# Kernel tuning notes

Hardware: AMD Instinct MI355X
Metric: run time of the kernel (lower is better)

Reference implementation:

```python
import jax, jax.numpy as jnp
import numpy as np

N_NODES = 50000
DIM = 128
N_EDGES = 800000
N_UID = 4096
ORDER = 3
LN_EPS = 1e-5


def setup_inputs() -> dict:
    key = jax.random.key(0)
    ks = jax.random.split(key, 6)
    scale = 1.0 / np.sqrt(DIM)
    embedding = jax.random.normal(ks[0], (N_NODES, DIM), jnp.float32) * np.sqrt(2.0 / DIM)  # kaiming-ish
    W = jax.random.normal(ks[1], (ORDER, DIM, DIM), jnp.float32) * scale
    b = jnp.zeros((ORDER, DIM), jnp.float32)
    gamma = jnp.ones((ORDER, DIM), jnp.float32)
    beta = jnp.zeros((ORDER, DIM), jnp.float32)
    src = jax.random.randint(ks[2], (N_EDGES,), 0, N_NODES, jnp.int32)
    dst = jax.random.randint(ks[3], (N_EDGES,), 0, N_NODES, jnp.int32)
    uid = jax.random.randint(ks[4], (N_UID,), 0, N_NODES, jnp.int32)
    return {"embedding": embedding, "W": W, "b": b, "gamma": gamma,
            "beta": beta, "src": src, "dst": dst, "uid": uid}


def _layer_norm(x, g, bta):
    mu = jnp.mean(x, axis=-1, keepdims=True)
    var = jnp.var(x, axis=-1, keepdims=True)
    return (x - mu) * jax.lax.rsqrt(var + LN_EPS) * g + bta


def reference(embedding, W, b, gamma, beta, src, dst, uid):
    # in-degree per destination node (DGL 'gcn' aggregator uses in_degrees)
    deg = jax.ops.segment_sum(jnp.ones((src.shape[0],), embedding.dtype), dst,
                              num_segments=N_NODES)  # [N]
    inv = (1.0 / (deg + 1.0))[:, None]  # [N,1]
    feats = embedding
    for i in range(ORDER):
        # gather source features, scatter-sum into destinations
        neigh = jax.ops.segment_sum(feats[src], dst, num_segments=N_NODES)  # [N,D]
        h = (neigh + feats) * inv                    # gcn-style mean incl. self
        h = jnp.einsum('nd,ed->ne', h, W[i]) + b[i]  # fc_neigh
        feats = jax.nn.elu(_layer_norm(h, gamma[i], beta[i]))
    return feats[uid]  # [N_UID, D]
```

## Files before the change

kernel.cpp:

```cpp
#include <hip/hip_runtime.h>
#include <math.h>

typedef unsigned int   uint;
typedef unsigned short ushort;

#define N_NODES 50000
#define DIM     128
#define N_EDGES 800000
#define N_UID   4096
#define LN_EPS  1e-5f
#define RST     132
#define XST     136
#define NBUCK   196
#define PCHUNK  4096
#define DBINS   128

typedef __attribute__((ext_vector_type(8))) short bf16x8;
typedef __attribute__((ext_vector_type(4))) float f32x4;
typedef __attribute__((ext_vector_type(4))) uint  u32x4;

__device__ __forceinline__ float bf_lo(uint u) { return __builtin_bit_cast(float, u << 16); }
__device__ __forceinline__ float bf_hi(uint u) { return __builtin_bit_cast(float, u & 0xffff0000u); }
__device__ __forceinline__ uint pack_bf16(float a, float b) {
    uint ua = __builtin_bit_cast(uint, a);
    uint ub = __builtin_bit_cast(uint, b);
    uint ra = (ua + 0x7fffu + ((ua >> 16) & 1u)) >> 16;
    uint rb = (ub + 0x7fffu + ((ub >> 16) & 1u)) >> 16;
    return ra | (rb << 16);
}

__global__ __launch_bounds__(256) void cvthist_kernel(const float* __restrict__ emb, ushort* __restrict__ E,
                                                      const float* __restrict__ W, ushort* __restrict__ WB,
                                                      const int* __restrict__ dst, int* __restrict__ bhist) {
    __shared__ int h[256];
    const int t = threadIdx.x;
    h[t] = 0;
    __syncthreads();
    const int gsz = gridDim.x * 256;
    for (int i = blockIdx.x * 256 + t; i < N_NODES * DIM / 4; i += gsz) {
        const float4 v = ((const float4*)emb)[i];
        uint2 p;
        p.x = pack_bf16(v.x, v.y);
        p.y = pack_bf16(v.z, v.w);
        ((uint2*)E)[i] = p;
    }
    {
        const int i = blockIdx.x * 256 + t;
        if (i < 3 * DIM * DIM / 4) {
            const float4 v = ((const float4*)W)[i];
            uint2 p;
            p.x = pack_bf16(v.x, v.y);
            p.y = pack_bf16(v.z, v.w);
            ((uint2*)WB)[i] = p;
        }
    }
    for (int e = blockIdx.x * 256 + t; e < N_EDGES; e += gsz)
        atomicAdd(&h[dst[e] >> 8], 1);
    __syncthreads();
    if (t < NBUCK && h[t]) atomicAdd(&bhist[t], h[t]);
}

__global__ __launch_bounds__(256) void part_kernel(const int* __restrict__ src, const int* __restrict__ dst,
                                                   const int* __restrict__ bhist, int* __restrict__ bcur,
                                                   int2* __restrict__ pak) {
    __shared__ int sc[256];
    __shared__ int h[256];
    __shared__ int base[256];
    __shared__ int cur[256];
    const int t = threadIdx.x;
    const int v = (t < NBUCK) ? bhist[t] : 0;
    sc[t] = v;
    h[t] = 0; cur[t] = 0;
    __syncthreads();
    for (int o = 1; o < 256; o <<= 1) {
        int x = (t >= o) ? sc[t - o] : 0;
        __syncthreads();
        sc[t] += x;
        __syncthreads();
    }
    const int excl = sc[t] - v;
    const int e0 = blockIdx.x * PCHUNK;
    const int e1 = min(e0 + PCHUNK, N_EDGES);
    for (int i = e0 + t; i < e1; i += 256)
        atomicAdd(&h[dst[i] >> 8], 1);
    __syncthreads();
    if (t < NBUCK && h[t]) base[t] = excl + atomicAdd(&bcur[t], h[t]);
    __syncthreads();
    for (int i = e0 + t; i < e1; i += 256) {
        const int s = src[i], d = dst[i];
        const int b = d >> 8;
        const int q = atomicAdd(&cur[b], 1);
        pak[base[b] + q] = make_int2(s, d);
    }
}

__global__ __launch_bounds__(256) void bucket_kernel(const int2* __restrict__ pak, const int* __restrict__ bhist,
                                                     int* __restrict__ off, int* __restrict__ csr,
                                                     int* __restrict__ dhist) {
    __shared__ int sc[256];
    __shared__ int cnt[256];
    __shared__ int pos[256];
    __shared__ int dh[DBINS];
    const int b = blockIdx.x, t = threadIdx.x;
    const int bv = (t < NBUCK) ? bhist[t] : 0;
    sc[t] = bv;
    cnt[t] = 0;
    if (t < DBINS) dh[t] = 0;
    __syncthreads();
    for (int o = 1; o < 256; o <<= 1) {
        int x = (t >= o) ? sc[t - o] : 0;
        __syncthreads();
        sc[t] += x;
        __syncthreads();
    }
    const int e0 = (b == 0) ? 0 : sc[b - 1];
    const int e1 = sc[b];
    const int m = e1 - e0;
    for (int i = t; i < m; i += 256) atomicAdd(&cnt[pak[e0 + i].y & 255], 1);
    __syncthreads();
    const int c = cnt[t];
    pos[t] = c;
    __syncthreads();
    for (int o = 1; o < 256; o <<= 1) {
        int x = (t >= o) ? pos[t - o] : 0;
        __syncthreads();
        pos[t] += x;
        __syncthreads();
    }
    const int excl = pos[t] - c;
    const int node = b * 256 + t;
    if (node < N_NODES) {
        off[node] = e0 + excl;
        atomicAdd(&dh[min(c, DBINS - 1)], 1);
    }
    if (b == 0 && t == 0) off[N_NODES] = N_EDGES;
    __syncthreads();
    if (t < DBINS && dh[t]) atomicAdd(&dhist[t], dh[t]);
    pos[t] = excl;
    __syncthreads();
    for (int i = t; i < m; i += 256) {
        const int2 p = pak[e0 + i];
        const int q = atomicAdd(&pos[p.y & 255], 1);
        csr[e0 + q] = p.x;
    }
}

__global__ __launch_bounds__(256) void dscat_kernel(const int* __restrict__ off, const int* __restrict__ dhist,
                                                    int* __restrict__ dcur, int* __restrict__ perm) {
    __shared__ int sc[DBINS];
    __shared__ int dv[DBINS];
    __shared__ int lh[DBINS];
    __shared__ int lbase[DBINS];
    __shared__ int lcur[DBINS];
    const int b = blockIdx.x, t = threadIdx.x;
    if (t < DBINS) { lh[t] = 0; lcur[t] = 0; }
    __syncthreads();
    const int node = b * 256 + t;
    int bin = -1;
    if (node < N_NODES) {
        const int deg = off[node + 1] - off[node];
        bin = min(deg, DBINS - 1);
        atomicAdd(&lh[bin], 1);
    }
    __syncthreads();
    if (t < DBINS) { dv[t] = dhist[t]; sc[t] = dv[t]; }
    __syncthreads();
    for (int o = 1; o < DBINS; o <<= 1) {
        int x = (t >= o && t < DBINS) ? sc[t - o] : 0;
        __syncthreads();
        if (t < DBINS) sc[t] += x;
        __syncthreads();
    }
    if (t < DBINS) {
        const int excl = sc[t] - dv[t];
        if (lh[t]) lbase[t] = excl + atomicAdd(&dcur[t], lh[t]);
    }
    __syncthreads();
    if (node < N_NODES) {
        const int q = atomicAdd(&lcur[bin], 1);
        perm[lbase[bin] + q] = node;
    }
}

template <bool OUT_BF16, bool PERMOUT>
__global__ __launch_bounds__(512) void layer_kernel(
    const ushort* __restrict__ fin, void* __restrict__ fout,
    const int* __restrict__ off, const int* __restrict__ csr,
    const int* __restrict__ nodemap, const ushort* __restrict__ wb,
    const float* __restrict__ bias, const float* __restrict__ gamma,
    const float* __restrict__ beta, int nrows)
{
    __shared__ ushort xs[32 * XST];
    __shared__ float  ys[32 * RST];
    __shared__ int    nid[32];
    const int t = threadIdx.x;
    const int rows = blockIdx.x * 32;

    {
        const int lx   = t & 15;
        const int st   = t >> 4;
        const int slot = rows + st;
        const bool valid = slot < nrows;
        const int n  = valid ? (nodemap ? nodemap[slot] : slot) : 0;
        if (lx == 0) nid[st] = n;
        const int d0 = off[n];
        int d1 = off[n + 1];
        if (!valid) d1 = d0;
        const int deg = d1 - d0;

        float a[8];
        {
            const uint4 q = ((const uint4*)(fin + (size_t)n * DIM))[lx];
            a[0]=bf_lo(q.x); a[1]=bf_hi(q.x); a[2]=bf_lo(q.y); a[3]=bf_hi(q.y);
            a[4]=bf_lo(q.z); a[5]=bf_hi(q.z); a[6]=bf_lo(q.w); a[7]=bf_hi(q.w);
        }

        const int nfull = deg >> 3;
        int e = d0;
        int id[8];
        if (nfull > 0) {
            #pragma unroll
            for (int k = 0; k < 8; ++k) id[k] = csr[e + k];
        }
        for (int r = 0; r < nfull; ++r) {
            uint4 v[8];
            #pragma unroll
            for (int k = 0; k < 8; ++k)
                v[k] = ((const uint4*)(fin + (size_t)id[k] * DIM))[lx];
            int idn[8];
            if (r + 1 < nfull) {
                #pragma unroll
                for (int k = 0; k < 8; ++k) idn[k] = csr[e + 8 + k];
            }
            #pragma unroll
            for (int k = 0; k < 8; ++k) {
                a[0] += bf_lo(v[k].x); a[1] += bf_hi(v[k].x);
                a[2] += bf_lo(v[k].y); a[3] += bf_hi(v[k].y);
                a[4] += bf_lo(v[k].z); a[5] += bf_hi(v[k].z);
                a[6] += bf_lo(v[k].w); a[7] += bf_hi(v[k].w);
            }
            if (r + 1 < nfull) {
                #pragma unroll
                for (int k = 0; k < 8; ++k) id[k] = idn[k];
            }
            e += 8;
        }
        if (e < d1) {
            const int last = d1 - 1;
            int   idt[8];
            float m[8];
            #pragma unroll
            for (int k = 0; k < 8; ++k) {
                const int ee = e + k;
                idt[k] = csr[(ee <= last) ? ee : last];
                m[k]   = (ee <= last) ? 1.0f : 0.0f;
            }
            uint4 v[8];
            #pragma unroll
            for (int k = 0; k < 8; ++k)
                v[k] = ((const uint4*)(fin + (size_t)idt[k] * DIM))[lx];
            #pragma unroll
            for (int k = 0; k < 8; ++k) {
                a[0] = fmaf(m[k], bf_lo(v[k].x), a[0]); a[1] = fmaf(m[k], bf_hi(v[k].x), a[1]);
                a[2] = fmaf(m[k], bf_lo(v[k].y), a[2]); a[3] = fmaf(m[k], bf_hi(v[k].y), a[3]);
                a[4] = fmaf(m[k], bf_lo(v[k].z), a[4]); a[5] = fmaf(m[k], bf_hi(v[k].z), a[5]);
                a[6] = fmaf(m[k], bf_lo(v[k].w), a[6]); a[7] = fmaf(m[k], bf_hi(v[k].w), a[7]);
            }
        }

        const float iv = 1.0f / (float)(deg + 1);
        uint4 p;
        p.x = pack_bf16(a[0] * iv, a[1] * iv);
        p.y = pack_bf16(a[2] * iv, a[3] * iv);
        p.z = pack_bf16(a[4] * iv, a[5] * iv);
        p.w = pack_bf16(a[6] * iv, a[7] * iv);
        *((uint4*)(xs + st * XST + lx * 8)) = p;
    }
    __syncthreads();

    {
        const int wave = t >> 6, lane = t & 63;
        const int row_off = (wave >> 2) * 16;
        const int col_off = (wave & 3) * 32;
        const int lm   = lane & 15;
        const int quad = lane >> 4;
        f32x4 acc[2] = {f32x4{0,0,0,0}, f32x4{0,0,0,0}};
        const ushort* xrow = xs + (row_off + lm) * XST + quad * 8;
        const ushort* __restrict__ wrow = wb + (size_t)(col_off + lm) * DIM + quad * 8;
        #pragma unroll
        for (int kk = 0; kk < 4; ++kk) {
            const bf16x8 af = __builtin_bit_cast(bf16x8, *(const u32x4*)(xrow + kk * 32));
            #pragma unroll
            for (int c = 0; c < 2; ++c) {
                const bf16x8 bf = __builtin_bit_cast(bf16x8,
                    *(const u32x4*)(wrow + (size_t)c * 16 * DIM + kk * 32));
                acc[c] = __builtin_amdgcn_mfma_f32_16x16x32_bf16(af, bf, acc[c], 0, 0, 0);
            }
        }
        #pragma unroll
        for (int c = 0; c < 2; ++c) {
            #pragma unroll
            for (int r = 0; r < 4; ++r)
                ys[(row_off + quad * 4 + r) * RST + col_off + c * 16 + lm] = acc[c][r];
        }
    }
    __syncthreads();

    {
        const int r   = t >> 4;
        const int seg = t & 15;
        const int db  = seg * 8;
        const float* yr = ys + r * RST + db;
        float vs[8];
        {
            const float4 y0 = ((const float4*)yr)[0];
            const float4 y1 = ((const float4*)yr)[1];
            const float4 b0 = ((const float4*)(bias + db))[0];
            const float4 b1 = ((const float4*)(bias + db))[1];
            vs[0] = y0.x + b0.x; vs[1] = y0.y + b0.y; vs[2] = y0.z + b0.z; vs[3] = y0.w + b0.w;
            vs[4] = y1.x + b1.x; vs[5] = y1.y + b1.y; vs[6] = y1.z + b1.z; vs[7] = y1.w + b1.w;
        }
        float s1 = 0.0f, s2 = 0.0f;
        #pragma unroll
        for (int i = 0; i < 8; ++i) { s1 += vs[i]; s2 += vs[i] * vs[i]; }
        #pragma unroll
        for (int m = 1; m < 16; m <<= 1) {
            s1 += __shfl_xor(s1, m);
            s2 += __shfl_xor(s2, m);
        }
        const float mu  = s1 * (1.0f / 128.0f);
        const float var = s2 * (1.0f / 128.0f) - mu * mu;
        const float rs  = rsqrtf(var + LN_EPS);
        float ov[8];
        {
            const float4 g0 = ((const float4*)(gamma + db))[0];
            const float4 g1 = ((const float4*)(gamma + db))[1];
            const float4 t0 = ((const float4*)(beta + db))[0];
            const float4 t1 = ((const float4*)(beta + db))[1];
            float z;
            z = (vs[0] - mu) * rs * g0.x + t0.x; ov[0] = (z > 0.0f) ? z : expm1f(z);
            z = (vs[1] - mu) * rs * g0.y + t0.y; ov[1] = (z > 0.0f) ? z : expm1f(z);
            z = (vs[2] - mu) * rs * g0.z + t0.z; ov[2] = (z > 0.0f) ? z : expm1f(z);
            z = (vs[3] - mu) * rs * g0.w + t0.w; ov[3] = (z > 0.0f) ? z : expm1f(z);
            z = (vs[4] - mu) * rs * g1.x + t1.x; ov[4] = (z > 0.0f) ? z : expm1f(z);
            z = (vs[5] - mu) * rs * g1.y + t1.y; ov[5] = (z > 0.0f) ? z : expm1f(z);
            z = (vs[6] - mu) * rs * g1.z + t1.z; ov[6] = (z > 0.0f) ? z : expm1f(z);
            z = (vs[7] - mu) * rs * g1.w + t1.w; ov[7] = (z > 0.0f) ? z : expm1f(z);
        }
        const int slot3 = rows + r;
        if (slot3 < nrows) {
            const int nout = PERMOUT ? nid[r] : slot3;
            if (OUT_BF16) {
                uint4 p;
                p.x = pack_bf16(ov[0], ov[1]);
                p.y = pack_bf16(ov[2], ov[3]);
                p.z = pack_bf16(ov[4], ov[5]);
                p.w = pack_bf16(ov[6], ov[7]);
                *((uint4*)((ushort*)fout + (size_t)nout * DIM + db)) = p;
            } else {
                float* op = (float*)fout + (size_t)nout * DIM + db;
                ((float4*)op)[0] = make_float4(ov[0], ov[1], ov[2], ov[3]);
                ((float4*)op)[1] = make_float4(ov[4], ov[5], ov[6], ov[7]);
            }
        }
    }
}

extern "C" void kernel_launch(void* const* d_in, const int* in_sizes, int n_in,
                              void* d_out, int out_size, void* d_ws, size_t ws_size,
                              hipStream_t stream) {
    const float* emb   = (const float*)d_in[0];
    const float* W     = (const float*)d_in[1];
    const float* bias  = (const float*)d_in[2];
    const float* gamma = (const float*)d_in[3];
    const float* beta  = (const float*)d_in[4];
    const int*   src   = (const int*)d_in[5];
    const int*   dst   = (const int*)d_in[6];
    const int*   uid   = (const int*)d_in[7];

    ushort* E     = (ushort*)d_ws;
    ushort* A     = E + (size_t)N_NODES * DIM;
    ushort* B     = A + (size_t)N_NODES * DIM;
    ushort* WB    = B + (size_t)N_NODES * DIM;
    int*    off   = (int*)(WB + 3 * DIM * DIM);
    int*    aux   = off + (N_NODES + 4);
    int*    bhist = aux;
    int*    bcur  = aux + 256;
    int*    dhist = aux + 512;
    int*    dcur  = aux + 640;
    int*    perm  = aux + 768;
    int2*   pak   = (int2*)(perm + N_NODES);
    int*    csr   = (int*)(pak + N_EDGES);

    hipMemsetAsync(aux, 0, 768 * sizeof(int), stream);
    cvthist_kernel<<<512, 256, 0, stream>>>(emb, E, W, WB, dst, bhist);
    part_kernel<<<(N_EDGES + PCHUNK - 1) / PCHUNK, 256, 0, stream>>>(src, dst, bhist, bcur, pak);
    bucket_kernel<<<NBUCK, 256, 0, stream>>>(pak, bhist, off, csr, dhist);
    dscat_kernel<<<NBUCK, 256, 0, stream>>>(off, dhist, dcur, perm);

    const int lblk = (N_NODES + 31) / 32;
    layer_kernel<true, true><<<lblk, 512, 0, stream>>>(E, A, off, csr, perm, WB,
                                                       bias, gamma, beta, N_NODES);
    layer_kernel<true, true><<<lblk, 512, 0, stream>>>(A, B, off, csr, perm, WB + DIM * DIM,
                                                       bias + DIM, gamma + DIM, beta + DIM, N_NODES);
    layer_kernel<false, false><<<N_UID / 32, 512, 0, stream>>>(B, (float*)d_out, off, csr, uid,
                                                               WB + 2 * DIM * DIM, bias + 2 * DIM,
                                                               gamma + 2 * DIM, beta + 2 * DIM, N_UID);
}
```

Measured before the change: 233.7 us.

## Replace degree-sorted node permutation with edge-balanced per-block aggregation

Drops the degree histogram and permutation kernel and processes nodes in natural order. Within each 32-node block, edges are split evenly across 32 sub-groups, each binary-searches its starting node and flushes partial sums into shared memory with atomics. This aims to remove the extra dscat launch and the scattered permuted reads and writes while still balancing per-row gather work. In exchange it adds LDS atomics, a zeroing pass and a binary search, and blocks whose nodes have very different degrees stay unbalanced against each other.

```diff
diff --git a/kernel.cpp b/kernel.cpp
--- a/kernel.cpp
+++ b/kernel.cpp
@@ -13,7 +13,6 @@
 #define XST     136
 #define NBUCK   196
 #define PCHUNK  4096
-#define DBINS   128
 
 typedef __attribute__((ext_vector_type(8))) short bf16x8;
 typedef __attribute__((ext_vector_type(4))) float f32x4;
@@ -95,17 +94,14 @@
 }
 
 __global__ __launch_bounds__(256) void bucket_kernel(const int2* __restrict__ pak, const int* __restrict__ bhist,
-                                                     int* __restrict__ off, int* __restrict__ csr,
-                                                     int* __restrict__ dhist) {
+                                                     int* __restrict__ off, int* __restrict__ csr) {
     __shared__ int sc[256];
     __shared__ int cnt[256];
     __shared__ int pos[256];
-    __shared__ int dh[DBINS];
     const int b = blockIdx.x, t = threadIdx.x;
     const int bv = (t < NBUCK) ? bhist[t] : 0;
     sc[t] = bv;
     cnt[t] = 0;
-    if (t < DBINS) dh[t] = 0;
     __syncthreads();
     for (int o = 1; o < 256; o <<= 1) {
         int x = (t >= o) ? sc[t - o] : 0;
@@ -129,13 +125,9 @@
     }
     const int excl = pos[t] - c;
     const int node = b * 256 + t;
-    if (node < N_NODES) {
-        off[node] = e0 + excl;
-        atomicAdd(&dh[min(c, DBINS - 1)], 1);
-    }
+    if (node < N_NODES) off[node] = e0 + excl;
     if (b == 0 && t == 0) off[N_NODES] = N_EDGES;
     __syncthreads();
-    if (t < DBINS && dh[t]) atomicAdd(&dhist[t], dh[t]);
     pos[t] = excl;
     __syncthreads();
     for (int i = t; i < m; i += 256) {
@@ -145,136 +137,94 @@
     }
 }
 
-__global__ __launch_bounds__(256) void dscat_kernel(const int* __restrict__ off, const int* __restrict__ dhist,
-                                                    int* __restrict__ dcur, int* __restrict__ perm) {
-    __shared__ int sc[DBINS];
-    __shared__ int dv[DBINS];
-    __shared__ int lh[DBINS];
-    __shared__ int lbase[DBINS];
-    __shared__ int lcur[DBINS];
-    const int b = blockIdx.x, t = threadIdx.x;
-    if (t < DBINS) { lh[t] = 0; lcur[t] = 0; }
-    __syncthreads();
-    const int node = b * 256 + t;
-    int bin = -1;
-    if (node < N_NODES) {
-        const int deg = off[node + 1] - off[node];
-        bin = min(deg, DBINS - 1);
-        atomicAdd(&lh[bin], 1);
-    }
-    __syncthreads();
-    if (t < DBINS) { dv[t] = dhist[t]; sc[t] = dv[t]; }
-    __syncthreads();
-    for (int o = 1; o < DBINS; o <<= 1) {
-        int x = (t >= o && t < DBINS) ? sc[t - o] : 0;
-        __syncthreads();
-        if (t < DBINS) sc[t] += x;
-        __syncthreads();
-    }
-    if (t < DBINS) {
-        const int excl = sc[t] - dv[t];
-        if (lh[t]) lbase[t] = excl + atomicAdd(&dcur[t], lh[t]);
-    }
-    __syncthreads();
-    if (node < N_NODES) {
-        const int q = atomicAdd(&lcur[bin], 1);
-        perm[lbase[bin] + q] = node;
-    }
-}
-
-template <bool OUT_BF16, bool PERMOUT>
-__global__ __launch_bounds__(512) void layer_kernel(
-    const ushort* __restrict__ fin, void* __restrict__ fout,
+__global__ __launch_bounds__(512) void layerbal_kernel(
+    const ushort* __restrict__ fin, ushort* __restrict__ fout,
     const int* __restrict__ off, const int* __restrict__ csr,
-    const int* __restrict__ nodemap, const ushort* __restrict__ wb,
-    const float* __restrict__ bias, const float* __restrict__ gamma,
-    const float* __restrict__ beta, int nrows)
+    const ushort* __restrict__ wb, const float* __restrict__ bias,
+    const float* __restrict__ gamma, const float* __restrict__ beta, int nrows)
 {
     __shared__ ushort xs[32 * XST];
     __shared__ float  ys[32 * RST];
-    __shared__ int    nid[32];
+    __shared__ int    noff[33];
     const int t = threadIdx.x;
     const int rows = blockIdx.x * 32;
-
-    {
-        const int lx   = t & 15;
-        const int st   = t >> 4;
-        const int slot = rows + st;
-        const bool valid = slot < nrows;
-        const int n  = valid ? (nodemap ? nodemap[slot] : slot) : 0;
-        if (lx == 0) nid[st] = n;
-        const int d0 = off[n];
-        int d1 = off[n + 1];
-        if (!valid) d1 = d0;
-        const int deg = d1 - d0;
-
-        float a[8];
-        {
-            const uint4 q = ((const uint4*)(fin + (size_t)n * DIM))[lx];
-            a[0]=bf_lo(q.x); a[1]=bf_hi(q.x); a[2]=bf_lo(q.y); a[3]=bf_hi(q.y);
-            a[4]=bf_lo(q.z); a[5]=bf_hi(q.z); a[6]=bf_lo(q.w); a[7]=bf_hi(q.w);
-        }
-
-        const int nfull = deg >> 3;
-        int e = d0;
-        int id[8];
-        if (nfull > 0) {
-            #pragma unroll
-            for (int k = 0; k < 8; ++k) id[k] = csr[e + k];
-        }
-        for (int r = 0; r < nfull; ++r) {
-            uint4 v[8];
-            #pragma unroll
-            for (int k = 0; k < 8; ++k)
-                v[k] = ((const uint4*)(fin + (size_t)id[k] * DIM))[lx];
-            int idn[8];
-            if (r + 1 < nfull) {
+    const int nvalid = min(32, nrows - rows);
+
+    for (int i = t; i < 32 * RST; i += 512) ys[i] = 0.0f;
+    if (t <= nvalid) noff[t] = off[rows + t];
+    __syncthreads();
+
+    {
+        const int lx = t & 15;
+        const int st = t >> 4;
+        const int e0 = noff[0], e1 = noff[nvalid];
+        const int per = ((e1 - e0) + 31) >> 5;
+        const int s0 = e0 + st * per;
+        const int s1 = min(s0 + per, e1);
+        if (s0 < s1) {
+            int lo = 0, hi = nvalid - 1;
+            while (lo < hi) {
+                const int mid = (lo + hi + 1) >> 1;
+                if (noff[mid] <= s0) lo = mid; else hi = mid - 1;
+            }
+            int p  = lo;
+            int nb = noff[p + 1];
+            float acc[8] = {0, 0, 0, 0, 0, 0, 0, 0};
+            for (int e = s0; e < s1; e += 8) {
+                const int cnt = min(8, s1 - e);
+                int id[8];
                 #pragma unroll
-                for (int k = 0; k < 8; ++k) idn[k] = csr[e + 8 + k];
-            }
-            #pragma unroll
-            for (int k = 0; k < 8; ++k) {
-                a[0] += bf_lo(v[k].x); a[1] += bf_hi(v[k].x);
-                a[2] += bf_lo(v[k].y); a[3] += bf_hi(v[k].y);
-                a[4] += bf_lo(v[k].z); a[5] += bf_hi(v[k].z);
-                a[6] += bf_lo(v[k].w); a[7] += bf_hi(v[k].w);
-            }
-            if (r + 1 < nfull) {
+                for (int k = 0; k < 8; ++k)
+                    id[k] = csr[(k < cnt) ? (e + k) : (s1 - 1)];
+                uint4 v[8];
                 #pragma unroll
-                for (int k = 0; k < 8; ++k) id[k] = idn[k];
-            }
-            e += 8;
-        }
-        if (e < d1) {
-            const int last = d1 - 1;
-            int   idt[8];
-            float m[8];
-            #pragma unroll
-            for (int k = 0; k < 8; ++k) {
-                const int ee = e + k;
-                idt[k] = csr[(ee <= last) ? ee : last];
-                m[k]   = (ee <= last) ? 1.0f : 0.0f;
-            }
-            uint4 v[8];
-            #pragma unroll
-            for (int k = 0; k < 8; ++k)
-                v[k] = ((const uint4*)(fin + (size_t)idt[k] * DIM))[lx];
-            #pragma unroll
-            for (int k = 0; k < 8; ++k) {
-                a[0] = fmaf(m[k], bf_lo(v[k].x), a[0]); a[1] = fmaf(m[k], bf_hi(v[k].x), a[1]);
-                a[2] = fmaf(m[k], bf_lo(v[k].y), a[2]); a[3] = fmaf(m[k], bf_hi(v[k].y), a[3]);
-                a[4] = fmaf(m[k], bf_lo(v[k].z), a[4]); a[5] = fmaf(m[k], bf_hi(v[k].z), a[5]);
-                a[6] = fmaf(m[k], bf_lo(v[k].w), a[6]); a[7] = fmaf(m[k], bf_hi(v[k].w), a[7]);
-            }
-        }
-
-        const float iv = 1.0f / (float)(deg + 1);
-        uint4 p;
-        p.x = pack_bf16(a[0] * iv, a[1] * iv);
-        p.y = pack_bf16(a[2] * iv, a[3] * iv);
-        p.z = pack_bf16(a[4] * iv, a[5] * iv);
-        p.w = pack_bf16(a[6] * iv, a[7] * iv);
-        *((uint4*)(xs + st * XST + lx * 8)) = p;
+                for (int k = 0; k < 8; ++k)
+                    v[k] = ((const uint4*)(fin + (size_t)id[k] * DIM))[lx];
+                #pragma unroll
+                for (int k = 0; k < 8; ++k) {
+                    if (k < cnt) {
+                        const int ee = e + k;
+                        while (ee >= nb) {
+                            float* yp = ys + p * RST + lx * 8;
+                            #pragma unroll
+                            for (int j = 0; j < 8; ++j) atomicAdd(&yp[j], acc[j]);
+                            #pragma unroll
+                            for (int j = 0; j < 8; ++j) acc[j] = 0.0f;
+                            ++p;
+                            nb = noff[p + 1];
+                        }
+                        acc[0] += bf_lo(v[k].x); acc[1] += bf_hi(v[k].x);
+                        acc[2] += bf_lo(v[k].y); acc[3] += bf_hi(v[k].y);
+                        acc[4] += bf_lo(v[k].z); acc[5] += bf_hi(v[k].z);
+                        acc[6] += bf_lo(v[k].w); acc[7] += bf_hi(v[k].w);
+                    }
+                }
+            }
+            float* yp = ys + p * RST + lx * 8;
+            #pragma unroll
+            for (int j = 0; j < 8; ++j) atomicAdd(&yp[j], acc[j]);
+        }
+    }
+    __syncthreads();
+
+    {
+        const int lx = t & 15;
+        const int st = t >> 4;
+        uint4 p4 = make_uint4(0, 0, 0, 0);
+        if (st < nvalid) {
+            const uint4 q = ((const uint4*)(fin + (size_t)(rows + st) * DIM))[lx];
+            const float* yr = ys + st * RST + lx * 8;
+            const float iv = 1.0f / (float)(noff[st + 1] - noff[st] + 1);
+            const float o0 = (yr[0] + bf_lo(q.x)) * iv, o1 = (yr[1] + bf_hi(q.x)) * iv;
+            const float o2 = (yr[2] + bf_lo(q.y)) * iv, o3 = (yr[3] + bf_hi(q.y)) * iv;
+            const float o4 = (yr[4] + bf_lo(q.z)) * iv, o5 = (yr[5] + bf_hi(q.z)) * iv;
+            const float o6 = (yr[6] + bf_lo(q.w)) * iv, o7 = (yr[7] + bf_hi(q.w)) * iv;
+            p4.x = pack_bf16(o0, o1);
+            p4.y = pack_bf16(o2, o3);
+            p4.z = pack_bf16(o4, o5);
+            p4.w = pack_bf16(o6, o7);
+        }
+        *((uint4*)(xs + st * XST + lx * 8)) = p4;
     }
     __syncthreads();
 
@@ -347,21 +297,183 @@
             z = (vs[6] - mu) * rs * g1.z + t1.z; ov[6] = (z > 0.0f) ? z : expm1f(z);
             z = (vs[7] - mu) * rs * g1.w + t1.w; ov[7] = (z > 0.0f) ? z : expm1f(z);
         }
-        const int slot3 = rows + r;
-        if (slot3 < nrows) {
-            const int nout = PERMOUT ? nid[r] : slot3;
-            if (OUT_BF16) {
-                uint4 p;
-                p.x = pack_bf16(ov[0], ov[1]);
-                p.y = pack_bf16(ov[2], ov[3]);
-                p.z = pack_bf16(ov[4], ov[5]);
-                p.w = pack_bf16(ov[6], ov[7]);
-                *((uint4*)((ushort*)fout + (size_t)nout * DIM + db)) = p;
-            } else {
-                float* op = (float*)fout + (size_t)nout * DIM + db;
-                ((float4*)op)[0] = make_float4(ov[0], ov[1], ov[2], ov[3]);
-                ((float4*)op)[1] = make_float4(ov[4], ov[5], ov[6], ov[7]);
-            }
+        const int n = rows + r;
+        if (n < nrows) {
+            uint4 p;
+            p.x = pack_bf16(ov[0], ov[1]);
+            p.y = pack_bf16(ov[2], ov[3]);
+            p.z = pack_bf16(ov[4], ov[5]);
+            p.w = pack_bf16(ov[6], ov[7]);
+            *((uint4*)(fout + (size_t)n * DIM + db)) = p;
+        }
+    }
+}
+
+__global__ __launch_bounds__(512) void layeruid_kernel(
+    const ushort* __restrict__ fin, float* __restrict__ fout,
+    const int* __restrict__ off, const int* __restrict__ csr,
+    const int* __restrict__ uidmap, const ushort* __restrict__ wb,
+    const float* __restrict__ bias, const float* __restrict__ gamma,
+    const float* __restrict__ beta, int nrows)
+{
+    __shared__ ushort xs[32 * XST];
+    __shared__ float  ys[32 * RST];
+    const int t = threadIdx.x;
+    const int rows = blockIdx.x * 32;
+
+    {
+        const int lx   = t & 15;
+        const int st   = t >> 4;
+        const int slot = rows + st;
+        const bool valid = slot < nrows;
+        const int n  = valid ? uidmap[slot] : 0;
+        const int d0 = off[n];
+        int d1 = off[n + 1];
+        if (!valid) d1 = d0;
+        const int deg = d1 - d0;
+
+        float a[8];
+        {
+            const uint4 q = ((const uint4*)(fin + (size_t)n * DIM))[lx];
+            a[0]=bf_lo(q.x); a[1]=bf_hi(q.x); a[2]=bf_lo(q.y); a[3]=bf_hi(q.y);
+            a[4]=bf_lo(q.z); a[5]=bf_hi(q.z); a[6]=bf_lo(q.w); a[7]=bf_hi(q.w);
+        }
+        const int nfull = deg >> 3;
+        int e = d0;
+        int id[8];
+        if (nfull > 0) {
+            #pragma unroll
+            for (int k = 0; k < 8; ++k) id[k] = csr[e + k];
+        }
+        for (int r = 0; r < nfull; ++r) {
+            uint4 v[8];
+            #pragma unroll
+            for (int k = 0; k < 8; ++k)
+                v[k] = ((const uint4*)(fin + (size_t)id[k] * DIM))[lx];
+            int idn[8];
+            if (r + 1 < nfull) {
+                #pragma unroll
+                for (int k = 0; k < 8; ++k) idn[k] = csr[e + 8 + k];
+            }
+            #pragma unroll
+            for (int k = 0; k < 8; ++k) {
+                a[0] += bf_lo(v[k].x); a[1] += bf_hi(v[k].x);
+                a[2] += bf_lo(v[k].y); a[3] += bf_hi(v[k].y);
+                a[4] += bf_lo(v[k].z); a[5] += bf_hi(v[k].z);
+                a[6] += bf_lo(v[k].w); a[7] += bf_hi(v[k].w);
+            }
+            if (r + 1 < nfull) {
+                #pragma unroll
+                for (int k = 0; k < 8; ++k) id[k] = idn[k];
+            }
+            e += 8;
+        }
+        if (e < d1) {
+            const int last = d1 - 1;
+            int   idt[8];
+            float m[8];
+            #pragma unroll
+            for (int k = 0; k < 8; ++k) {
+                const int ee = e + k;
+                idt[k] = csr[(ee <= last) ? ee : last];
+                m[k]   = (ee <= last) ? 1.0f : 0.0f;
+            }
+            uint4 v[8];
+            #pragma unroll
+            for (int k = 0; k < 8; ++k)
+                v[k] = ((const uint4*)(fin + (size_t)idt[k] * DIM))[lx];
+            #pragma unroll
+            for (int k = 0; k < 8; ++k) {
+                a[0] = fmaf(m[k], bf_lo(v[k].x), a[0]); a[1] = fmaf(m[k], bf_hi(v[k].x), a[1]);
+                a[2] = fmaf(m[k], bf_lo(v[k].y), a[2]); a[3] = fmaf(m[k], bf_hi(v[k].y), a[3]);
+                a[4] = fmaf(m[k], bf_lo(v[k].z), a[4]); a[5] = fmaf(m[k], bf_hi(v[k].z), a[5]);
+                a[6] = fmaf(m[k], bf_lo(v[k].w), a[6]); a[7] = fmaf(m[k], bf_hi(v[k].w), a[7]);
+            }
+        }
+        const float iv = 1.0f / (float)(deg + 1);
+        uint4 p;
+        p.x = pack_bf16(a[0] * iv, a[1] * iv);
+        p.y = pack_bf16(a[2] * iv, a[3] * iv);
+        p.z = pack_bf16(a[4] * iv, a[5] * iv);
+        p.w = pack_bf16(a[6] * iv, a[7] * iv);
+        *((uint4*)(xs + st * XST + lx * 8)) = p;
+    }
+    __syncthreads();
+
+    {
+        const int wave = t >> 6, lane = t & 63;
+        const int row_off = (wave >> 2) * 16;
+        const int col_off = (wave & 3) * 32;
+        const int lm   = lane & 15;
+        const int quad = lane >> 4;
+        f32x4 acc[2] = {f32x4{0,0,0,0}, f32x4{0,0,0,0}};
+        const ushort* xrow = xs + (row_off + lm) * XST + quad * 8;
+        const ushort* __restrict__ wrow = wb + (size_t)(col_off + lm) * DIM + quad * 8;
+        #pragma unroll
+        for (int kk = 0; kk < 4; ++kk) {
+            const bf16x8 af = __builtin_bit_cast(bf16x8, *(const u32x4*)(xrow + kk * 32));
+            #pragma unroll
+            for (int c = 0; c < 2; ++c) {
+                const bf16x8 bf = __builtin_bit_cast(bf16x8,
+                    *(const u32x4*)(wrow + (size_t)c * 16 * DIM + kk * 32));
+                acc[c] = __builtin_amdgcn_mfma_f32_16x16x32_bf16(af, bf, acc[c], 0, 0, 0);
+            }
+        }
+        #pragma unroll
+        for (int c = 0; c < 2; ++c) {
+            #pragma unroll
+            for (int r = 0; r < 4; ++r)
+                ys[(row_off + quad * 4 + r) * RST + col_off + c * 16 + lm] = acc[c][r];
+        }
+    }
+    __syncthreads();
+
+    {
+        const int r   = t >> 4;
+        const int seg = t & 15;
+        const int db  = seg * 8;
+        const float* yr = ys + r * RST + db;
+        float vs[8];
+        {
+            const float4 y0 = ((const float4*)yr)[0];
+            const float4 y1 = ((const float4*)yr)[1];
+            const float4 b0 = ((const float4*)(bias + db))[0];
+            const float4 b1 = ((const float4*)(bias + db))[1];
+            vs[0] = y0.x + b0.x; vs[1] = y0.y + b0.y; vs[2] = y0.z + b0.z; vs[3] = y0.w + b0.w;
+            vs[4] = y1.x + b1.x; vs[5] = y1.y + b1.y; vs[6] = y1.z + b1.z; vs[7] = y1.w + b1.w;
+        }
+        float s1 = 0.0f, s2 = 0.0f;
+        #pragma unroll
+        for (int i = 0; i < 8; ++i) { s1 += vs[i]; s2 += vs[i] * vs[i]; }
+        #pragma unroll
+        for (int m = 1; m < 16; m <<= 1) {
+            s1 += __shfl_xor(s1, m);
+            s2 += __shfl_xor(s2, m);
+        }
+        const float mu  = s1 * (1.0f / 128.0f);
+        const float var = s2 * (1.0f / 128.0f) - mu * mu;
+        const float rs  = rsqrtf(var + LN_EPS);
+        float ov[8];
+        {
+            const float4 g0 = ((const float4*)(gamma + db))[0];
+            const float4 g1 = ((const float4*)(gamma + db))[1];
+            const float4 t0 = ((const float4*)(beta + db))[0];
+            const float4 t1 = ((const float4*)(beta + db))[1];
+            float z;
+            z = (vs[0] - mu) * rs * g0.x + t0.x; ov[0] = (z > 0.0f) ? z : expm1f(z);
+            z = (vs[1] - mu) * rs * g0.y + t0.y; ov[1] = (z > 0.0f) ? z : expm1f(z);
+            z = (vs[2] - mu) * rs * g0.z + t0.z; ov[2] = (z > 0.0f) ? z : expm1f(z);
+            z = (vs[3] - mu) * rs * g0.w + t0.w; ov[3] = (z > 0.0f) ? z : expm1f(z);
+            z = (vs[4] - mu) * rs * g1.x + t1.x; ov[4] = (z > 0.0f) ? z : expm1f(z);
+            z = (vs[5] - mu) * rs * g1.y + t1.y; ov[5] = (z > 0.0f) ? z : expm1f(z);
+            z = (vs[6] - mu) * rs * g1.z + t1.z; ov[6] = (z > 0.0f) ? z : expm1f(z);
+            z = (vs[7] - mu) * rs * g1.w + t1.w; ov[7] = (z > 0.0f) ? z : expm1f(z);
+        }
+        const int slot = rows + r;
+        if (slot < nrows) {
+            float* op = fout + (size_t)slot * DIM + db;
+            ((float4*)op)[0] = make_float4(ov[0], ov[1], ov[2], ov[3]);
+            ((float4*)op)[1] = make_float4(ov[4], ov[5], ov[6], ov[7]);
         }
     }
 }
@@ -386,24 +498,20 @@
     int*    aux   = off + (N_NODES + 4);
     int*    bhist = aux;
     int*    bcur  = aux + 256;
-    int*    dhist = aux + 512;
-    int*    dcur  = aux + 640;
-    int*    perm  = aux + 768;
-    int2*   pak   = (int2*)(perm + N_NODES);
+    int2*   pak   = (int2*)(aux + 512);
     int*    csr   = (int*)(pak + N_EDGES);
 
-    hipMemsetAsync(aux, 0, 768 * sizeof(int), stream);
+    hipMemsetAsync(aux, 0, 512 * sizeof(int), stream);
     cvthist_kernel<<<512, 256, 0, stream>>>(emb, E, W, WB, dst, bhist);
     part_kernel<<<(N_EDGES + PCHUNK - 1) / PCHUNK, 256, 0, stream>>>(src, dst, bhist, bcur, pak);
-    bucket_kernel<<<NBUCK, 256, 0, stream>>>(pak, bhist, off, csr, dhist);
-    dscat_kernel<<<NBUCK, 256, 0, stream>>>(off, dhist, dcur, perm);
+    bucket_kernel<<<NBUCK, 256, 0, stream>>>(pak, bhist, off, csr);
 
     const int lblk = (N_NODES + 31) / 32;
-    layer_kernel<true, true><<<lblk, 512, 0, stream>>>(E, A, off, csr, perm, WB,
-                                                       bias, gamma, beta, N_NODES);
-    layer_kernel<true, true><<<lblk, 512, 0, stream>>>(A, B, off, csr, perm, WB + DIM * DIM,
-                                                       bias + DIM, gamma + DIM, beta + DIM, N_NODES);
-    layer_kernel<false, false><<<N_UID / 32, 512, 0, stream>>>(B, (float*)d_out, off, csr, uid,
-                                                               WB + 2 * DIM * DIM, bias + 2 * DIM,
-                                                               gamma + 2 * DIM, beta + 2 * DIM, N_UID);
-}
+    layerbal_kernel<<<lblk, 512, 0, stream>>>(E, A, off, csr, WB,
+                                              bias, gamma, beta, N_NODES);
+    layerbal_kernel<<<lblk, 512, 0, stream>>>(A, B, off, csr, WB + DIM * DIM,
+                                              bias + DIM, gamma + DIM, beta + DIM, N_NODES);
+    layeruid_kernel<<<N_UID / 32, 512, 0, stream>>>(B, (float*)d_out, off, csr, uid,
+                                                    WB + 2 * DIM * DIM, bias + 2 * DIM,
+                                                    gamma + 2 * DIM, beta + 2 * DIM, N_UID);
+}
```

Result: slower. 319.0 us (+36.5%).

## Drop degree-sorted node permutation and pack edge pairs into 32-bit words

Applied to the files above, without the earlier changes.

Removes the degree-histogram/scatter kernel and the permutation of nodes by in-degree, so the two full layers process nodes in natural order. Edge pairs in the partition buffer are packed as 16-bit source plus low 8 bits of destination in one 32-bit word, halving that intermediate traffic. This saves a launch and memory traffic in preprocessing but gives up the per-block degree balancing in the aggregation layers. The packing relies on node ids fitting in 16 bits.

```diff
diff --git a/kernel.cpp b/kernel.cpp
--- a/kernel.cpp
+++ b/kernel.cpp
@@ -13,7 +13,6 @@
 #define XST     136
 #define NBUCK   196
 #define PCHUNK  4096
-#define DBINS   128
 
 typedef __attribute__((ext_vector_type(8))) short bf16x8;
 typedef __attribute__((ext_vector_type(4))) float f32x4;
@@ -62,7 +61,7 @@
 
 __global__ __launch_bounds__(256) void part_kernel(const int* __restrict__ src, const int* __restrict__ dst,
                                                    const int* __restrict__ bhist, int* __restrict__ bcur,
-                                                   int2* __restrict__ pak) {
+                                                   uint* __restrict__ pak) {
     __shared__ int sc[256];
     __shared__ int h[256];
     __shared__ int base[256];
@@ -90,22 +89,19 @@
         const int s = src[i], d = dst[i];
         const int b = d >> 8;
         const int q = atomicAdd(&cur[b], 1);
-        pak[base[b] + q] = make_int2(s, d);
-    }
-}
-
-__global__ __launch_bounds__(256) void bucket_kernel(const int2* __restrict__ pak, const int* __restrict__ bhist,
-                                                     int* __restrict__ off, int* __restrict__ csr,
-                                                     int* __restrict__ dhist) {
+        pak[base[b] + q] = (uint)s | ((uint)(d & 255) << 16);
+    }
+}
+
+__global__ __launch_bounds__(256) void bucket_kernel(const uint* __restrict__ pak, const int* __restrict__ bhist,
+                                                     int* __restrict__ off, int* __restrict__ csr) {
     __shared__ int sc[256];
     __shared__ int cnt[256];
     __shared__ int pos[256];
-    __shared__ int dh[DBINS];
     const int b = blockIdx.x, t = threadIdx.x;
     const int bv = (t < NBUCK) ? bhist[t] : 0;
     sc[t] = bv;
     cnt[t] = 0;
-    if (t < DBINS) dh[t] = 0;
     __syncthreads();
     for (int o = 1; o < 256; o <<= 1) {
         int x = (t >= o) ? sc[t - o] : 0;
@@ -116,7 +112,7 @@
     const int e0 = (b == 0) ? 0 : sc[b - 1];
     const int e1 = sc[b];
     const int m = e1 - e0;
-    for (int i = t; i < m; i += 256) atomicAdd(&cnt[pak[e0 + i].y & 255], 1);
+    for (int i = t; i < m; i += 256) atomicAdd(&cnt[(pak[e0 + i] >> 16) & 255], 1);
     __syncthreads();
     const int c = cnt[t];
     pos[t] = c;
@@ -129,60 +125,19 @@
     }
     const int excl = pos[t] - c;
     const int node = b * 256 + t;
-    if (node < N_NODES) {
-        off[node] = e0 + excl;
-        atomicAdd(&dh[min(c, DBINS - 1)], 1);
-    }
+    if (node < N_NODES) off[node] = e0 + excl;
     if (b == 0 && t == 0) off[N_NODES] = N_EDGES;
     __syncthreads();
-    if (t < DBINS && dh[t]) atomicAdd(&dhist[t], dh[t]);
     pos[t] = excl;
     __syncthreads();
     for (int i = t; i < m; i += 256) {
-        const int2 p = pak[e0 + i];
-        const int q = atomicAdd(&pos[p.y & 255], 1);
-        csr[e0 + q] = p.x;
-    }
-}
-
-__global__ __launch_bounds__(256) void dscat_kernel(const int* __restrict__ off, const int* __restrict__ dhist,
-                                                    int* __restrict__ dcur, int* __restrict__ perm) {
-    __shared__ int sc[DBINS];
-    __shared__ int dv[DBINS];
-    __shared__ int lh[DBINS];
-    __shared__ int lbase[DBINS];
-    __shared__ int lcur[DBINS];
-    const int b = blockIdx.x, t = threadIdx.x;
-    if (t < DBINS) { lh[t] = 0; lcur[t] = 0; }
-    __syncthreads();
-    const int node = b * 256 + t;
-    int bin = -1;
-    if (node < N_NODES) {
-        const int deg = off[node + 1] - off[node];
-        bin = min(deg, DBINS - 1);
-        atomicAdd(&lh[bin], 1);
-    }
-    __syncthreads();
-    if (t < DBINS) { dv[t] = dhist[t]; sc[t] = dv[t]; }
-    __syncthreads();
-    for (int o = 1; o < DBINS; o <<= 1) {
-        int x = (t >= o && t < DBINS) ? sc[t - o] : 0;
-        __syncthreads();
-        if (t < DBINS) sc[t] += x;
-        __syncthreads();
-    }
-    if (t < DBINS) {
-        const int excl = sc[t] - dv[t];
-        if (lh[t]) lbase[t] = excl + atomicAdd(&dcur[t], lh[t]);
-    }
-    __syncthreads();
-    if (node < N_NODES) {
-        const int q = atomicAdd(&lcur[bin], 1);
-        perm[lbase[bin] + q] = node;
-    }
-}
-
-template <bool OUT_BF16, bool PERMOUT>
+        const uint p = pak[e0 + i];
+        const int q = atomicAdd(&pos[(p >> 16) & 255], 1);
+        csr[e0 + q] = (int)(p & 0xFFFFu);
+    }
+}
+
+template <bool OUT_BF16>
 __global__ __launch_bounds__(512) void layer_kernel(
     const ushort* __restrict__ fin, void* __restrict__ fout,
     const int* __restrict__ off, const int* __restrict__ csr,
@@ -192,7 +147,6 @@
 {
     __shared__ ushort xs[32 * XST];
     __shared__ float  ys[32 * RST];
-    __shared__ int    nid[32];
     const int t = threadIdx.x;
     const int rows = blockIdx.x * 32;
 
@@ -202,7 +156,6 @@
         const int slot = rows + st;
         const bool valid = slot < nrows;
         const int n  = valid ? (nodemap ? nodemap[slot] : slot) : 0;
-        if (lx == 0) nid[st] = n;
         const int d0 = off[n];
         int d1 = off[n + 1];
         if (!valid) d1 = d0;
@@ -347,18 +300,17 @@
             z = (vs[6] - mu) * rs * g1.z + t1.z; ov[6] = (z > 0.0f) ? z : expm1f(z);
             z = (vs[7] - mu) * rs * g1.w + t1.w; ov[7] = (z > 0.0f) ? z : expm1f(z);
         }
-        const int slot3 = rows + r;
-        if (slot3 < nrows) {
-            const int nout = PERMOUT ? nid[r] : slot3;
+        const int n = rows + r;
+        if (n < nrows) {
             if (OUT_BF16) {
                 uint4 p;
                 p.x = pack_bf16(ov[0], ov[1]);
                 p.y = pack_bf16(ov[2], ov[3]);
                 p.z = pack_bf16(ov[4], ov[5]);
                 p.w = pack_bf16(ov[6], ov[7]);
-                *((uint4*)((ushort*)fout + (size_t)nout * DIM + db)) = p;
+                *((uint4*)((ushort*)fout + (size_t)n * DIM + db)) = p;
             } else {
-                float* op = (float*)fout + (size_t)nout * DIM + db;
+                float* op = (float*)fout + (size_t)n * DIM + db;
                 ((float4*)op)[0] = make_float4(ov[0], ov[1], ov[2], ov[3]);
                 ((float4*)op)[1] = make_float4(ov[4], ov[5], ov[6], ov[7]);
             }
@@ -386,24 +338,20 @@
     int*    aux   = off + (N_NODES + 4);
     int*    bhist = aux;
     int*    bcur  = aux + 256;
-    int*    dhist = aux + 512;
-    int*    dcur  = aux + 640;
-    int*    perm  = aux + 768;
-    int2*   pak   = (int2*)(perm + N_NODES);
+    uint*   pak   = (uint*)(aux + 512);
     int*    csr   = (int*)(pak + N_EDGES);
 
-    hipMemsetAsync(aux, 0, 768 * sizeof(int), stream);
+    hipMemsetAsync(aux, 0, 512 * sizeof(int), stream);
     cvthist_kernel<<<512, 256, 0, stream>>>(emb, E, W, WB, dst, bhist);
     part_kernel<<<(N_EDGES + PCHUNK - 1) / PCHUNK, 256, 0, stream>>>(src, dst, bhist, bcur, pak);
-    bucket_kernel<<<NBUCK, 256, 0, stream>>>(pak, bhist, off, csr, dhist);
-    dscat_kernel<<<NBUCK, 256, 0, stream>>>(off, dhist, dcur, perm);
+    bucket_kernel<<<NBUCK, 256, 0, stream>>>(pak, bhist, off, csr);
 
     const int lblk = (N_NODES + 31) / 32;
-    layer_kernel<true, true><<<lblk, 512, 0, stream>>>(E, A, off, csr, perm, WB,
-                                                       bias, gamma, beta, N_NODES);
-    layer_kernel<true, true><<<lblk, 512, 0, stream>>>(A, B, off, csr, perm, WB + DIM * DIM,
-                                                       bias + DIM, gamma + DIM, beta + DIM, N_NODES);
-    layer_kernel<false, false><<<N_UID / 32, 512, 0, stream>>>(B, (float*)d_out, off, csr, uid,
-                                                               WB + 2 * DIM * DIM, bias + 2 * DIM,
-                                                               gamma + 2 * DIM, beta + 2 * DIM, N_UID);
-}
+    layer_kernel<true><<<lblk, 512, 0, stream>>>(E, A, off, csr, nullptr, WB,
+                                                 bias, gamma, beta, N_NODES);
+    layer_kernel<true><<<lblk, 512, 0, stream>>>(A, B, off, csr, nullptr, WB + DIM * DIM,
+                                                 bias + DIM, gamma + DIM, beta + DIM, N_NODES);
+    layer_kernel<false><<<N_UID / 32, 512, 0, stream>>>(B, (float*)d_out, off, csr, uid,
+                                                        WB + 2 * DIM * DIM, bias + 2 * DIM,
+                                                        gamma + 2 * DIM, beta + 2 * DIM, N_UID);
+}
```

Measured after the change: 230.5 us. About the same (-1.4%).
